# Kernel optimization log

Hardware: AMD Instinct MI355X
Metric: run time of the kernel (lower is better)

The kernel has to match this reference:

```python
import jax, jax.numpy as jnp
import numpy as np

B, L, D, H, T = 64, 512, 768, 384, 9  # batch, seq_len, hidden, hidden//2, num_tags


def setup_inputs() -> dict:
    key = jax.random.key(0)
    ks = jax.random.split(key, 8)
    return {
        "encoder_out": jax.random.normal(ks[0], (B, L, D), jnp.float32),
        "ner_labels": jax.random.randint(ks[1], (B, L), 0, T),
        "mask": jnp.ones((B, L), jnp.bool_),
        "W1": jax.random.normal(ks[2], (D, H), jnp.float32) / np.sqrt(D).astype(np.float32),
        "b1": jnp.zeros((H,), jnp.float32),
        "W2": jax.random.normal(ks[3], (H, T), jnp.float32) / np.sqrt(H).astype(np.float32),
        "b2": jnp.zeros((T,), jnp.float32),
        "start_trans": jax.random.uniform(ks[4], (T,), jnp.float32, -0.1, 0.1),
        "end_trans": jax.random.uniform(ks[5], (T,), jnp.float32, -0.1, 0.1),
        "trans": jax.random.uniform(ks[6], (T, T), jnp.float32, -0.1, 0.1),
    }


def _crf_nll(emissions, tags, mask, start_trans, end_trans, trans):
    """-mean log-likelihood, matching pytorch-crf forward (reduction='mean')."""
    maskf = mask.astype(emissions.dtype)
    # ---- numerator: score of the gold tag path ----
    emit = jnp.take_along_axis(emissions, tags[..., None], axis=-1)[..., 0]  # [B,L]
    emit_score = jnp.sum(emit * maskf, axis=1)
    tr = trans[tags[:, :-1], tags[:, 1:]]  # [B,L-1]
    tr_score = jnp.sum(tr * maskf[:, 1:], axis=1)
    last_idx = jnp.sum(mask.astype(jnp.int32), axis=1) - 1
    last_tags = jnp.take_along_axis(tags, last_idx[:, None], axis=1)[:, 0]
    numer = start_trans[tags[:, 0]] + emit_score + tr_score + end_trans[last_tags]
    # ---- denominator: forward algorithm (log partition) via scan ----
    alpha0 = start_trans[None, :] + emissions[:, 0]          # [B,T]
    em_rest = jnp.swapaxes(emissions[:, 1:], 0, 1)           # [L-1,B,T]
    mk_rest = jnp.swapaxes(maskf[:, 1:], 0, 1)               # [L-1,B]

    def step(alpha, xs):
        e_t, m_t = xs
        nxt = jax.nn.logsumexp(alpha[:, :, None] + trans[None, :, :] + e_t[:, None, :], axis=1)
        return jnp.where(m_t[:, None] > 0, nxt, alpha), None

    alpha, _ = jax.lax.scan(step, alpha0, (em_rest, mk_rest))
    denom = jax.nn.logsumexp(alpha + end_trans[None, :], axis=1)
    return -jnp.mean(numer - denom)


def reference(encoder_out, ner_labels, mask, W1, b1, W2, b2, start_trans, end_trans, trans):
    # proj: Linear -> GELU (exact erf, torch default) -> Dropout (identity in eval)
    h = jax.nn.gelu(encoder_out @ W1 + b1, approximate=False)
    emissions = h @ W2 + b2  # [B,L,T]
    return _crf_nll(emissions, ner_labels, mask, start_trans, end_trans, trans)
```

## Files before the change

kernel.cpp:

```cpp
#include <hip/hip_runtime.h>
#include <hip/hip_bf16.h>
#include <math.h>

#define B_ 64
#define L_ 512
#define D_ 768
#define H_ 384
#define T_ 9
#define M_ (B_ * L_)

typedef __attribute__((ext_vector_type(8))) short short8;
typedef __attribute__((ext_vector_type(4))) float f32x4;

__device__ __forceinline__ unsigned short f2bf(float f) {
    unsigned u = __float_as_uint(f);
    u += 0x7FFFu + ((u >> 16) & 1u);
    return (unsigned short)(u >> 16);
}

__device__ __forceinline__ unsigned pkbf2(float a, float b) {
    __hip_bfloat162 h = __float22bfloat162_rn(float2{a, b});
    return *(unsigned*)&h;
}

__device__ __forceinline__ float gelu_fast(float x) {
    float z2 = 1.5957691216f * x + 0.0713548162726f * x * x * x;
    return x / (1.f + __expf(-z2));
}

__device__ __forceinline__ float wredf(float v) {
#pragma unroll
    for (int m = 32; m >= 1; m >>= 1) v += __shfl_xor(v, m, 64);
    return v;
}

__device__ __forceinline__ void sync_lds() {
    asm volatile("s_waitcnt lgkmcnt(0)\n\ts_barrier" ::: "memory");
}

__global__ __launch_bounds__(256) void prep_kernel(
    const float* __restrict__ W1, const float* __restrict__ W2,
    unsigned short* __restrict__ W1F, unsigned short* __restrict__ W2F,
    float* __restrict__ out)
{
    if (blockIdx.x == 0 && threadIdx.x == 0) out[0] = 0.f;
    const int g    = blockIdx.x * 4 + (threadIdx.x >> 6);
    const int lane = threadIdx.x & 63;
    const int lm   = lane & 15;
    const int q    = lane >> 4;
    if (g < 576) {
        const int nt = g / 24;
        const int kc = g - nt * 24;
        const int n  = nt * 16 + lm;
        short8 v;
#pragma unroll
        for (int j = 0; j < 8; ++j)
            v[j] = (short)f2bf(W1[(size_t)(kc * 32 + q * 8 + j) * H_ + n]);
        *(short8*)(W1F + ((size_t)g * 64 + lane) * 8) = v;
    } else if (g < 588) {
        const int kk = g - 576;
        short8 v;
#pragma unroll
        for (int j = 0; j < 8; ++j) {
            int k = kk * 32 + q * 8 + j;
            v[j] = (lm < 9) ? (short)f2bf(W2[(size_t)k * T_ + lm]) : (short)0;
        }
        *(short8*)(W2F + ((size_t)kk * 64 + lane) * 8) = v;
    }
}

__global__ __launch_bounds__(512, 4) void emis_mfma_kernel(
    const float* __restrict__ X,
    const unsigned short* __restrict__ W1F,
    const float* __restrict__ b1,
    const unsigned short* __restrict__ W2F,
    const float* __restrict__ b2,
    float* __restrict__ em)
{
    __shared__ __align__(16) unsigned short Hs[64 * 392];
    char* smem = (char*)Hs;

    const int t    = threadIdx.x;
    const int lane = t & 63;
    const int w    = t >> 6;
    const int lm   = lane & 15;
    const int q    = lane >> 4;
    const int row0 = blockIdx.x * 64;

    const int srow   = t >> 3;
    const int slot8  = t & 7;
    const int schunk = (slot8 >> 1) ^ ((srow >> 1) & 3);
    const float* sp  = X + (size_t)(row0 + srow) * D_ + slot8 * 4;
    char* swr = smem + srow * 64 + schunk * 16 + (slot8 & 1) * 8;

    const int cq = (q ^ ((lm >> 1) & 3)) << 4;

    const unsigned short* wb = W1F + (size_t)(w * 3) * 12288 + lane * 8;

    f32x4 acc[4][3];
#pragma unroll
    for (int mt = 0; mt < 4; ++mt)
#pragma unroll
        for (int i = 0; i < 3; ++i) acc[mt][i] = (f32x4)0.f;

    short8 bb0[3], bb1[3], bb2[3];
    f32x4 g0, g1, g2;

#define LOADBB(dst, KC)                                                     \
    do {                                                                    \
        dst[0] = *(const short8*)(wb + 0 * 12288 + (KC) * 512);             \
        dst[1] = *(const short8*)(wb + 1 * 12288 + (KC) * 512);             \
        dst[2] = *(const short8*)(wb + 2 * 12288 + (KC) * 512);             \
    } while (0)

#define STWR(G, BUF)                                                        \
    do {                                                                    \
        int2 v2 = {(int)pkbf2(G[0], G[1]), (int)pkbf2(G[2], G[3])};         \
        *(int2*)(swr + (BUF) * 4096) = v2;                                  \
    } while (0)

    g0 = *(const f32x4*)(sp);
    STWR(g0, 0);
    g1 = *(const f32x4*)(sp + 32);
    g2 = *(const f32x4*)(sp + 64);
    LOADBB(bb0, 0);
    LOADBB(bb1, 1);
    sync_lds();

#define KSTEP(KC, BBc, BBn, Gn, Gw)                                         \
    do {                                                                    \
        if ((KC) + 3 <= 23) Gn = *(const f32x4*)(sp + ((KC) + 3) * 32);     \
        if ((KC) + 2 <= 23) { LOADBB(BBn, (KC) + 2); }                      \
        {                                                                   \
            const char* fb = smem + ((KC) & 1) * 4096;                      \
            short8 af0 = *(const short8*)(fb + ( 0 + lm) * 64 + cq);        \
            short8 af1 = *(const short8*)(fb + (16 + lm) * 64 + cq);        \
            short8 af2 = *(const short8*)(fb + (32 + lm) * 64 + cq);        \
            short8 af3 = *(const short8*)(fb + (48 + lm) * 64 + cq);        \
            acc[0][0] = __builtin_amdgcn_mfma_f32_16x16x32_bf16(af0, BBc[0], acc[0][0], 0, 0, 0); \
            acc[0][1] = __builtin_amdgcn_mfma_f32_16x16x32_bf16(af0, BBc[1], acc[0][1], 0, 0, 0); \
            acc[0][2] = __builtin_amdgcn_mfma_f32_16x16x32_bf16(af0, BBc[2], acc[0][2], 0, 0, 0); \
            acc[1][0] = __builtin_amdgcn_mfma_f32_16x16x32_bf16(af1, BBc[0], acc[1][0], 0, 0, 0); \
            acc[1][1] = __builtin_amdgcn_mfma_f32_16x16x32_bf16(af1, BBc[1], acc[1][1], 0, 0, 0); \
            acc[1][2] = __builtin_amdgcn_mfma_f32_16x16x32_bf16(af1, BBc[2], acc[1][2], 0, 0, 0); \
            acc[2][0] = __builtin_amdgcn_mfma_f32_16x16x32_bf16(af2, BBc[0], acc[2][0], 0, 0, 0); \
            acc[2][1] = __builtin_amdgcn_mfma_f32_16x16x32_bf16(af2, BBc[1], acc[2][1], 0, 0, 0); \
            acc[2][2] = __builtin_amdgcn_mfma_f32_16x16x32_bf16(af2, BBc[2], acc[2][2], 0, 0, 0); \
            acc[3][0] = __builtin_amdgcn_mfma_f32_16x16x32_bf16(af3, BBc[0], acc[3][0], 0, 0, 0); \
            acc[3][1] = __builtin_amdgcn_mfma_f32_16x16x32_bf16(af3, BBc[1], acc[3][1], 0, 0, 0); \
            acc[3][2] = __builtin_amdgcn_mfma_f32_16x16x32_bf16(af3, BBc[2], acc[3][2], 0, 0, 0); \
        }                                                                   \
        if ((KC) + 1 <= 23) {                                               \
            STWR(Gw, ((KC) + 1) & 1);                                       \
            sync_lds();                                                     \
        }                                                                   \
    } while (0)

    KSTEP(  0,  bb0, bb2, g0, g1);
    KSTEP(  1,  bb1, bb0, g1, g2);
    KSTEP(  2,  bb2, bb1, g2, g0);
    KSTEP(  3,  bb0, bb2, g0, g1);
    KSTEP(  4,  bb1, bb0, g1, g2);
    KSTEP(  5,  bb2, bb1, g2, g0);
    KSTEP(  6,  bb0, bb2, g0, g1);
    KSTEP(  7,  bb1, bb0, g1, g2);
    KSTEP(  8,  bb2, bb1, g2, g0);
    KSTEP(  9,  bb0, bb2, g0, g1);
    KSTEP( 10,  bb1, bb0, g1, g2);
    KSTEP( 11,  bb2, bb1, g2, g0);
    KSTEP( 12,  bb0, bb2, g0, g1);
    KSTEP( 13,  bb1, bb0, g1, g2);
    KSTEP( 14,  bb2, bb1, g2, g0);
    KSTEP( 15,  bb0, bb2, g0, g1);
    KSTEP( 16,  bb1, bb0, g1, g2);
    KSTEP( 17,  bb2, bb1, g2, g0);
    KSTEP( 18,  bb0, bb2, g0, g1);
    KSTEP( 19,  bb1, bb0, g1, g2);
    KSTEP( 20,  bb2, bb1, g2, g0);
    KSTEP( 21,  bb0, bb2, g0, g1);
    KSTEP( 22,  bb1, bb0, g1, g2);
    KSTEP( 23,  bb2, bb1, g2, g0);

#undef KSTEP
#undef LOADBB
#undef STWR

    __syncthreads();

#pragma unroll
    for (int i = 0; i < 3; ++i) {
        const int lc = w * 48 + i * 16 + lm;
        const float b1v = b1[lc];
#pragma unroll
        for (int mt = 0; mt < 4; ++mt)
#pragma unroll
            for (int r = 0; r < 4; ++r) {
                float h = gelu_fast(acc[mt][i][r] + b1v);
                Hs[(mt * 16 + q * 4 + r) * 392 + lc] = f2bf(h);
            }
    }
    __syncthreads();

    if (w < 4) {
        f32x4 e = (f32x4)0.f;
#pragma unroll
        for (int kk = 0; kk < 12; ++kk) {
            short8 ah = *(const short8*)&Hs[(w * 16 + lm) * 392 + kk * 32 + (q << 3)];
            short8 bw = *(const short8*)(W2F + ((size_t)(kk * 64 + lane)) * 8);
            e = __builtin_amdgcn_mfma_f32_16x16x32_bf16(ah, bw, e, 0, 0, 0);
        }
        if (lm < 9) {
#pragma unroll
            for (int r = 0; r < 4; ++r)
                em[(size_t)(row0 + w * 16 + q * 4 + r) * T_ + lm] = e[r] + b2[lm];
        }
    }
}

__global__ __launch_bounds__(640) void crf_kernel(
    const float* __restrict__ em,
    const int* __restrict__ labels,
    const unsigned char* __restrict__ maskb,
    const float* __restrict__ st,
    const float* __restrict__ et,
    const float* __restrict__ tr,
    float* __restrict__ out)
{
    const int b = blockIdx.x;
    const int t = threadIdx.x;

    __shared__ float es[64 * 73];
    __shared__ float Msa[64 * 81];
    __shared__ float Msb[32 * 81];
    __shared__ float trs[81];
    __shared__ float red_num;
    __shared__ unsigned char msh[L_];
    __shared__ int lbs[L_];

    const int mstride =
        (maskb[0] != 0 && maskb[1] == 0 && maskb[2] == 0 && maskb[3] == 0) ? 4 : 1;

    const float* e0 = em + (size_t)b * L_ * T_;
    for (int i = t; i < L_ * T_; i += 640) {
        int tt = i / T_, j = i - tt * T_;
        es[(tt >> 3) * 73 + (tt & 7) * 9 + j] = e0[i];
    }
    if (t < 81) trs[t] = tr[t];
    for (int i = t; i < L_; i += 640) {
        msh[i] = maskb[((size_t)b * L_ + i) * (size_t)mstride];
        lbs[i] = labels[b * L_ + i];
    }
    __syncthreads();

    if (t < 576) {
        const int c  = t / 9;
        const int i0 = t - c * 9;
        float trr[81];
#pragma unroll
        for (int i = 0; i < 81; ++i) trr[i] = trs[i];
        float V[9];
#pragma unroll
        for (int j = 0; j < 9; ++j) V[j] = (j == i0) ? 0.f : -1e30f;

        const int sbeg = (c == 0) ? 1 : 0;
        for (int s = sbeg; s < 8; ++s) {
            int tt = c * 8 + s;
            if (msh[tt]) {
                const float* ep = &es[c * 73 + s * 9];
                float nv[9];
#pragma unroll
                for (int j = 0; j < 9; ++j) {
                    float a[9];
#pragma unroll
                    for (int k = 0; k < 9; ++k) a[k] = V[k] + trr[k * 9 + j];
                    float mx = a[0];
#pragma unroll
                    for (int k = 1; k < 9; ++k) mx = fmaxf(mx, a[k]);
                    float sum = 0.f;
#pragma unroll
                    for (int k = 0; k < 9; ++k) sum += __expf(a[k] - mx);
                    nv[j] = ep[j] + mx + __logf(sum);
                }
#pragma unroll
                for (int j = 0; j < 9; ++j) V[j] = nv[j];
            }
        }
#pragma unroll
        for (int j = 0; j < 9; ++j) Msa[c * 81 + i0 * 9 + j] = V[j];
    } else {
        const int lane = t - 576;
        float emit_s = 0.f, tr_sc = 0.f, mcnt = 0.f;
        for (int tt = lane; tt < L_; tt += 64) {
            if (msh[tt]) {
                mcnt += 1.f;
                int tag = lbs[tt];
                emit_s += es[(tt >> 3) * 73 + (tt & 7) * 9 + tag];
                if (tt >= 1) tr_sc += trs[lbs[tt - 1] * 9 + tag];
            }
        }
        emit_s = wredf(emit_s);
        tr_sc  = wredf(tr_sc);
        mcnt   = wredf(mcnt);
        if (lane == 0) {
            int last = (int)mcnt - 1;
            red_num = st[lbs[0]] + emit_s + tr_sc + et[lbs[last]];
        }
    }
    __syncthreads();

    float* src = Msa;
    float* dst = Msb;
    for (int n = 32; n >= 1; n >>= 1) {
        for (int idx = t; idx < n * 81; idx += 640) {
            int p = idx / 81;
            int r = idx - p * 81;
            int i = r / 9, j = r - i * 9;
            const float* A  = src + (2 * p) * 81 + i * 9;
            const float* Bm = src + (2 * p + 1) * 81 + j;
            float v[9];
#pragma unroll
            for (int k = 0; k < 9; ++k) v[k] = A[k] + Bm[k * 9];
            float mx = v[0];
#pragma unroll
            for (int k = 1; k < 9; ++k) mx = fmaxf(mx, v[k]);
            float sum = 0.f;
#pragma unroll
            for (int k = 0; k < 9; ++k) sum += __expf(v[k] - mx);
            dst[p * 81 + r] = mx + __logf(sum);
        }
        __syncthreads();
        float* tmp = src; src = dst; dst = tmp;
    }

    if (t < 64) {
        float v = -3.0e38f;
        if (t < 9) {
            float a[9];
#pragma unroll
            for (int i = 0; i < 9; ++i) a[i] = st[i] + es[i] + src[i * 9 + t];
            float mx = a[0];
#pragma unroll
            for (int i = 1; i < 9; ++i) mx = fmaxf(mx, a[i]);
            float sum = 0.f;
#pragma unroll
            for (int i = 0; i < 9; ++i) sum += __expf(a[i] - mx);
            v = mx + __logf(sum) + et[t];
        }
        float mx = v;
#pragma unroll
        for (int m = 32; m >= 1; m >>= 1) mx = fmaxf(mx, __shfl_xor(mx, m, 64));
        float sm = __expf(v - mx);
        sm = wredf(sm);
        if (t == 0) {
            float denom = mx + __logf(sm);
            atomicAdd(out, (denom - red_num) * (1.0f / (float)B_));
        }
    }
}

extern "C" void kernel_launch(void* const* d_in, const int* in_sizes, int n_in,
                              void* d_out, int out_size, void* d_ws, size_t ws_size,
                              hipStream_t stream) {
    const float*         enc    = (const float*)d_in[0];
    const int*           labels = (const int*)d_in[1];
    const unsigned char* mask   = (const unsigned char*)d_in[2];
    const float*         W1     = (const float*)d_in[3];
    const float*         b1     = (const float*)d_in[4];
    const float*         W2     = (const float*)d_in[5];
    const float*         b2     = (const float*)d_in[6];
    const float*         st     = (const float*)d_in[7];
    const float*         et     = (const float*)d_in[8];
    const float*         tr     = (const float*)d_in[9];

    float* em           = (float*)d_ws;
    unsigned short* W1F = (unsigned short*)(em + (size_t)M_ * T_);
    unsigned short* W2F = W1F + (size_t)576 * 64 * 8;

    prep_kernel<<<147, 256, 0, stream>>>(W1, W2, W1F, W2F, (float*)d_out);
    emis_mfma_kernel<<<512, 512, 0, stream>>>(enc, W1F, b1, W2F, b2, em);
    crf_kernel<<<B_, 640, 0, stream>>>(em, labels, mask, st, et, tr, (float*)d_out);
}
```

Before: 223.3 us.

## Shrink emission GEMM tile to 32 rows with 4 waves covering 96 columns each

The fused Linear-GELU-Linear emission kernel now processes 32 rows per block with 256 threads instead of 64 rows with 512 threads. Each wave computes a 32x96 output tile instead of 64x48, and the grid doubles to 1024 blocks. W1 fragment prefetch drops from a triple to a double buffer, now one k-step ahead, and LDS use is halved. The goal is more blocks for better load balance and occupancy across CUs, at the cost of reading W1 fragments twice as often overall and a shallower prefetch that may expose more load latency.

```diff
diff --git a/kernel.cpp b/kernel.cpp
--- a/kernel.cpp
+++ b/kernel.cpp
@@ -69,7 +69,7 @@
     }
 }
 
-__global__ __launch_bounds__(512, 4) void emis_mfma_kernel(
+__global__ __launch_bounds__(256, 4) void emis_mfma_kernel(
     const float* __restrict__ X,
     const unsigned short* __restrict__ W1F,
     const float* __restrict__ b1,
@@ -77,7 +77,7 @@
     const float* __restrict__ b2,
     float* __restrict__ em)
 {
-    __shared__ __align__(16) unsigned short Hs[64 * 392];
+    __shared__ __align__(16) unsigned short Hs[32 * 392];
     char* smem = (char*)Hs;
 
     const int t    = threadIdx.x;
@@ -85,7 +85,7 @@
     const int w    = t >> 6;
     const int lm   = lane & 15;
     const int q    = lane >> 4;
-    const int row0 = blockIdx.x * 64;
+    const int row0 = blockIdx.x * 32;
 
     const int srow   = t >> 3;
     const int slot8  = t & 7;
@@ -95,15 +95,15 @@
 
     const int cq = (q ^ ((lm >> 1) & 3)) << 4;
 
-    const unsigned short* wb = W1F + (size_t)(w * 3) * 12288 + lane * 8;
-
-    f32x4 acc[4][3];
-#pragma unroll
-    for (int mt = 0; mt < 4; ++mt)
-#pragma unroll
-        for (int i = 0; i < 3; ++i) acc[mt][i] = (f32x4)0.f;
-
-    short8 bb0[3], bb1[3], bb2[3];
+    const unsigned short* wb = W1F + (size_t)(w * 6) * 12288 + lane * 8;
+
+    f32x4 acc[2][6];
+#pragma unroll
+    for (int mt = 0; mt < 2; ++mt)
+#pragma unroll
+        for (int i = 0; i < 6; ++i) acc[mt][i] = (f32x4)0.f;
+
+    short8 bb0[6], bb1[6];
     f32x4 g0, g1, g2;
 
 #define LOADBB(dst, KC)                                                     \
@@ -111,12 +111,15 @@
         dst[0] = *(const short8*)(wb + 0 * 12288 + (KC) * 512);             \
         dst[1] = *(const short8*)(wb + 1 * 12288 + (KC) * 512);             \
         dst[2] = *(const short8*)(wb + 2 * 12288 + (KC) * 512);             \
+        dst[3] = *(const short8*)(wb + 3 * 12288 + (KC) * 512);             \
+        dst[4] = *(const short8*)(wb + 4 * 12288 + (KC) * 512);             \
+        dst[5] = *(const short8*)(wb + 5 * 12288 + (KC) * 512);             \
     } while (0)
 
 #define STWR(G, BUF)                                                        \
     do {                                                                    \
         int2 v2 = {(int)pkbf2(G[0], G[1]), (int)pkbf2(G[2], G[3])};         \
-        *(int2*)(swr + (BUF) * 4096) = v2;                                  \
+        *(int2*)(swr + (BUF) * 2048) = v2;                                  \
     } while (0)
 
     g0 = *(const f32x4*)(sp);
@@ -124,31 +127,28 @@
     g1 = *(const f32x4*)(sp + 32);
     g2 = *(const f32x4*)(sp + 64);
     LOADBB(bb0, 0);
-    LOADBB(bb1, 1);
     sync_lds();
 
 #define KSTEP(KC, BBc, BBn, Gn, Gw)                                         \
     do {                                                                    \
         if ((KC) + 3 <= 23) Gn = *(const f32x4*)(sp + ((KC) + 3) * 32);     \
-        if ((KC) + 2 <= 23) { LOADBB(BBn, (KC) + 2); }                      \
+        if ((KC) + 1 <= 23) { LOADBB(BBn, (KC) + 1); }                      \
         {                                                                   \
-            const char* fb = smem + ((KC) & 1) * 4096;                      \
+            const char* fb = smem + ((KC) & 1) * 2048;                      \
             short8 af0 = *(const short8*)(fb + ( 0 + lm) * 64 + cq);        \
             short8 af1 = *(const short8*)(fb + (16 + lm) * 64 + cq);        \
-            short8 af2 = *(const short8*)(fb + (32 + lm) * 64 + cq);        \
-            short8 af3 = *(const short8*)(fb + (48 + lm) * 64 + cq);        \
             acc[0][0] = __builtin_amdgcn_mfma_f32_16x16x32_bf16(af0, BBc[0], acc[0][0], 0, 0, 0); \
             acc[0][1] = __builtin_amdgcn_mfma_f32_16x16x32_bf16(af0, BBc[1], acc[0][1], 0, 0, 0); \
             acc[0][2] = __builtin_amdgcn_mfma_f32_16x16x32_bf16(af0, BBc[2], acc[0][2], 0, 0, 0); \
+            acc[0][3] = __builtin_amdgcn_mfma_f32_16x16x32_bf16(af0, BBc[3], acc[0][3], 0, 0, 0); \
+            acc[0][4] = __builtin_amdgcn_mfma_f32_16x16x32_bf16(af0, BBc[4], acc[0][4], 0, 0, 0); \
+            acc[0][5] = __builtin_amdgcn_mfma_f32_16x16x32_bf16(af0, BBc[5], acc[0][5], 0, 0, 0); \
             acc[1][0] = __builtin_amdgcn_mfma_f32_16x16x32_bf16(af1, BBc[0], acc[1][0], 0, 0, 0); \
             acc[1][1] = __builtin_amdgcn_mfma_f32_16x16x32_bf16(af1, BBc[1], acc[1][1], 0, 0, 0); \
             acc[1][2] = __builtin_amdgcn_mfma_f32_16x16x32_bf16(af1, BBc[2], acc[1][2], 0, 0, 0); \
-            acc[2][0] = __builtin_amdgcn_mfma_f32_16x16x32_bf16(af2, BBc[0], acc[2][0], 0, 0, 0); \
-            acc[2][1] = __builtin_amdgcn_mfma_f32_16x16x32_bf16(af2, BBc[1], acc[2][1], 0, 0, 0); \
-            acc[2][2] = __builtin_amdgcn_mfma_f32_16x16x32_bf16(af2, BBc[2], acc[2][2], 0, 0, 0); \
-            acc[3][0] = __builtin_amdgcn_mfma_f32_16x16x32_bf16(af3, BBc[0], acc[3][0], 0, 0, 0); \
-            acc[3][1] = __builtin_amdgcn_mfma_f32_16x16x32_bf16(af3, BBc[1], acc[3][1], 0, 0, 0); \
-            acc[3][2] = __builtin_amdgcn_mfma_f32_16x16x32_bf16(af3, BBc[2], acc[3][2], 0, 0, 0); \
+            acc[1][3] = __builtin_amdgcn_mfma_f32_16x16x32_bf16(af1, BBc[3], acc[1][3], 0, 0, 0); \
+            acc[1][4] = __builtin_amdgcn_mfma_f32_16x16x32_bf16(af1, BBc[4], acc[1][4], 0, 0, 0); \
+            acc[1][5] = __builtin_amdgcn_mfma_f32_16x16x32_bf16(af1, BBc[5], acc[1][5], 0, 0, 0); \
         }                                                                   \
         if ((KC) + 1 <= 23) {                                               \
             STWR(Gw, ((KC) + 1) & 1);                                       \
@@ -156,30 +156,30 @@
         }                                                                   \
     } while (0)
 
-    KSTEP(  0,  bb0, bb2, g0, g1);
+    KSTEP(  0,  bb0, bb1, g0, g1);
     KSTEP(  1,  bb1, bb0, g1, g2);
-    KSTEP(  2,  bb2, bb1, g2, g0);
-    KSTEP(  3,  bb0, bb2, g0, g1);
-    KSTEP(  4,  bb1, bb0, g1, g2);
-    KSTEP(  5,  bb2, bb1, g2, g0);
-    KSTEP(  6,  bb0, bb2, g0, g1);
+    KSTEP(  2,  bb0, bb1, g2, g0);
+    KSTEP(  3,  bb1, bb0, g0, g1);
+    KSTEP(  4,  bb0, bb1, g1, g2);
+    KSTEP(  5,  bb1, bb0, g2, g0);
+    KSTEP(  6,  bb0, bb1, g0, g1);
     KSTEP(  7,  bb1, bb0, g1, g2);
-    KSTEP(  8,  bb2, bb1, g2, g0);
-    KSTEP(  9,  bb0, bb2, g0, g1);
-    KSTEP( 10,  bb1, bb0, g1, g2);
-    KSTEP( 11,  bb2, bb1, g2, g0);
-    KSTEP( 12,  bb0, bb2, g0, g1);
+    KSTEP(  8,  bb0, bb1, g2, g0);
+    KSTEP(  9,  bb1, bb0, g0, g1);
+    KSTEP( 10,  bb0, bb1, g1, g2);
+    KSTEP( 11,  bb1, bb0, g2, g0);
+    KSTEP( 12,  bb0, bb1, g0, g1);
     KSTEP( 13,  bb1, bb0, g1, g2);
-    KSTEP( 14,  bb2, bb1, g2, g0);
-    KSTEP( 15,  bb0, bb2, g0, g1);
-    KSTEP( 16,  bb1, bb0, g1, g2);
-    KSTEP( 17,  bb2, bb1, g2, g0);
-    KSTEP( 18,  bb0, bb2, g0, g1);
+    KSTEP( 14,  bb0, bb1, g2, g0);
+    KSTEP( 15,  bb1, bb0, g0, g1);
+    KSTEP( 16,  bb0, bb1, g1, g2);
+    KSTEP( 17,  bb1, bb0, g2, g0);
+    KSTEP( 18,  bb0, bb1, g0, g1);
     KSTEP( 19,  bb1, bb0, g1, g2);
-    KSTEP( 20,  bb2, bb1, g2, g0);
-    KSTEP( 21,  bb0, bb2, g0, g1);
-    KSTEP( 22,  bb1, bb0, g1, g2);
-    KSTEP( 23,  bb2, bb1, g2, g0);
+    KSTEP( 20,  bb0, bb1, g2, g0);
+    KSTEP( 21,  bb1, bb0, g0, g1);
+    KSTEP( 22,  bb0, bb1, g1, g2);
+    KSTEP( 23,  bb1, bb0, g2, g0);
 
 #undef KSTEP
 #undef LOADBB
@@ -188,11 +188,11 @@
     __syncthreads();
 
 #pragma unroll
-    for (int i = 0; i < 3; ++i) {
-        const int lc = w * 48 + i * 16 + lm;
+    for (int i = 0; i < 6; ++i) {
+        const int lc = w * 96 + i * 16 + lm;
         const float b1v = b1[lc];
 #pragma unroll
-        for (int mt = 0; mt < 4; ++mt)
+        for (int mt = 0; mt < 2; ++mt)
 #pragma unroll
             for (int r = 0; r < 4; ++r) {
                 float h = gelu_fast(acc[mt][i][r] + b1v);
@@ -201,7 +201,7 @@
     }
     __syncthreads();
 
-    if (w < 4) {
+    if (w < 2) {
         f32x4 e = (f32x4)0.f;
 #pragma unroll
         for (int kk = 0; kk < 12; ++kk) {
@@ -377,6 +377,6 @@
     unsigned short* W2F = W1F + (size_t)576 * 64 * 8;
 
     prep_kernel<<<147, 256, 0, stream>>>(W1, W2, W1F, W2F, (float*)d_out);
-    emis_mfma_kernel<<<512, 512, 0, stream>>>(enc, W1F, b1, W2F, b2, em);
+    emis_mfma_kernel<<<1024, 256, 0, stream>>>(enc, W1F, b1, W2F, b2, em);
     crf_kernel<<<B_, 640, 0, stream>>>(em, labels, mask, st, et, tr, (float*)d_out);
 }
```

Measured after the change: 243.5 us. +9.0%, slower.
